# Optimization experiments

Measured on AMD Instinct MI355X. Metric: run time of the kernel, lower is better.

## Reference

```python
import jax, jax.numpy as jnp
import numpy as np

B, S, D = 2048, 200, 192  # batch, seq_len, total_dim
H1, H2 = 64, 32
IN = 4 * D


def prelu(x, a):
    return jnp.where(x >= 0, x, a * x)


def setup_inputs() -> dict:
    key = jax.random.key(0)
    ks = jax.random.split(key, 10)
    scale = lambda fan_in: 1.0 / np.sqrt(fan_in)
    return {
        "query": jax.random.normal(ks[0], (B, D), jnp.float32),
        "keys": jax.random.normal(ks[1], (B, S, D), jnp.float32),
        "keys_mask": jax.random.randint(ks[2], (B, S), 0, 2, jnp.int32),
        "W1": jax.random.uniform(ks[3], (IN, H1), jnp.float32, -scale(IN), scale(IN)),
        "b1": jnp.zeros((H1,), jnp.float32),
        "a1": jnp.asarray(0.25, jnp.float32),  # PReLU default slope
        "W2": jax.random.uniform(ks[4], (H1, H2), jnp.float32, -scale(H1), scale(H1)),
        "b2": jnp.zeros((H2,), jnp.float32),
        "a2": jnp.asarray(0.25, jnp.float32),
        "W3": jax.random.uniform(ks[5], (H2, 1), jnp.float32, -scale(H2), scale(H2)),
        "b3": jnp.zeros((1,), jnp.float32),
    }


def reference(query, keys, keys_mask, W1, b1, a1, W2, b2, a2, W3, b3):
    q = query[:, None, :]  # [B,1,D] broadcasts against keys [B,S,D]
    qe = jnp.broadcast_to(q, keys.shape)
    x = jnp.concatenate([keys, qe, keys * qe, keys - qe], axis=-1)  # [B,S,4D]
    h = prelu(jnp.einsum("bsi,ih->bsh", x, W1) + b1, a1)
    h = prelu(jnp.einsum("bsh,hk->bsk", h, W2) + b2, a2)
    scores = (jnp.einsum("bsk,ko->bso", h, W3) + b3)[..., 0]  # [B,S]
    scores = jnp.where(keys_mask.astype(bool), scores, -jnp.inf)
    w = jax.nn.softmax(scores, axis=-1)
    w = jnp.where(jnp.isnan(w), jnp.zeros_like(w), w)
    weighted_sum = jnp.einsum("bs,bsd->bd", w, keys)
    return weighted_sum, w
```

## Files before the change

kernel.cpp:

```cpp
#include <hip/hip_runtime.h>


#define B_N 2048
#define S_N 200
#define D_N 192

typedef __bf16 bf16x8 __attribute__((ext_vector_type(8)));
typedef __bf16 bf16x4 __attribute__((ext_vector_type(4)));
typedef float  f32x4  __attribute__((ext_vector_type(4)));

struct __align__(16) Smem {
  unsigned char kbuf[64*400];
  unsigned char h1buf[64*144];
  unsigned char w2t[32*144];
  float qbuf[192];
  float cbuf[64];
  float cpart[4][64];
  float scores[256];
  int   maskbuf[256];
  float opart[4][192];
  float wm[4], wl[4];
  float w3buf[32];
  float b2buf[32];
  float consts[4];
};

__global__ __launch_bounds__(256, 3) void rich_attn_kernel(
    const float* __restrict__ query, const float* __restrict__ keys,
    const int*   __restrict__ keys_mask, const float* __restrict__ W1,
    const float* __restrict__ b1, const float* __restrict__ a1,
    const float* __restrict__ W2, const float* __restrict__ b2,
    const float* __restrict__ a2, const float* __restrict__ W3,
    const float* __restrict__ b3, float* __restrict__ out)
{
  __shared__ Smem sm;
  const int tid  = threadIdx.x;
  const int b    = blockIdx.x;
  const int wave = tid >> 6;
  const int lane = tid & 63;
  const int quad = (tid >> 4) & 3;
  const int n16  = tid & 15;

  if (tid < 192) sm.qbuf[tid] = query[b*D_N + tid];
  sm.maskbuf[tid] = (tid < 200) ? keys_mask[b*S_N + tid] : 0;
  if (tid < 32)  sm.w3buf[tid] = W3[tid];
  else if (tid < 64) sm.b2buf[tid-32] = b2[tid-32];
  if (tid == 64) { sm.consts[0] = a1[0]; sm.consts[1] = a2[0]; sm.consts[2] = b3[0]; }
  for (int i = tid; i < 64*32; i += 256) {
    int hh = i >> 5, kk = i & 31;
    *((__bf16*)&sm.w2t[kk*144 + hh*2]) = (__bf16)W2[i];
  }
  __syncthreads();

  {
    int hh = tid & 63, pp = tid >> 6;
    float acc = 0.f;
    int d0 = pp*48;
    #pragma unroll 4
    for (int d = d0; d < d0+48; ++d)
      acc += sm.qbuf[d] * (W1[(192+d)*64 + hh] - W1[(576+d)*64 + hh]);
    sm.cpart[pp][hh] = acc;
  }
  bf16x8 fb1[6];
  {
    int h = (wave << 4) | n16;
    #pragma unroll
    for (int t = 0; t < 6; ++t) {
      #pragma unroll
      for (int j = 0; j < 8; ++j) {
        int d = t*32 + quad*8 + j;
        float v = W1[d*64 + h] + W1[(576+d)*64 + h] + sm.qbuf[d]*W1[(384+d)*64 + h];
        fb1[t][j] = (__bf16)v;
      }
    }
  }
  bf16x8 fw2[2][2];
  #pragma unroll
  for (int nt2 = 0; nt2 < 2; ++nt2)
    #pragma unroll
    for (int t = 0; t < 2; ++t)
      fw2[nt2][t] = *(const bf16x8*)&sm.w2t[(nt2*16 + n16)*144 + (t*32 + quad*8)*2];
  const float w3v0 = sm.w3buf[n16],      w3v1 = sm.w3buf[16 + n16];
  const float bbv0 = sm.b2buf[n16],      bbv1 = sm.b2buf[16 + n16];
  const float a1v = sm.consts[0], a2v = sm.consts[1], b3v = sm.consts[2];
  __syncthreads();
  if (tid < 64)
    sm.cbuf[tid] = b1[tid] + sm.cpart[0][tid] + sm.cpart[1][tid]
                 + sm.cpart[2][tid] + sm.cpart[3][tid];

  const float* kb = keys + (size_t)b * (S_N * D_N);
  float m_run = -1e30f, l_run = 0.f;
  f32x4 o = {0.f, 0.f, 0.f, 0.f};

  for (int tile = 0; tile < 4; ++tile) {
    const int s0 = tile * 64;
    #pragma unroll
    for (int i = 0; i < 12; ++i) {
      int f = tid + i*256;
      int row = f / 48, c4 = f % 48;
      int sg = s0 + row;
      float4 v = make_float4(0.f, 0.f, 0.f, 0.f);
      if (sg < 200) v = ((const float4*)kb)[sg*48 + c4];
      bf16x4 bv; bv[0]=(__bf16)v.x; bv[1]=(__bf16)v.y; bv[2]=(__bf16)v.z; bv[3]=(__bf16)v.w;
      *(bf16x4*)&sm.kbuf[row*400 + c4*8] = bv;
    }
    __syncthreads();

    f32x4 acc1[4];
    #pragma unroll
    for (int mt = 0; mt < 4; ++mt) acc1[mt] = (f32x4){0.f,0.f,0.f,0.f};
    #pragma unroll
    for (int mt = 0; mt < 4; ++mt)
      #pragma unroll
      for (int t = 0; t < 6; ++t) {
        bf16x8 fa = *(const bf16x8*)&sm.kbuf[(mt*16 + n16)*400 + (t*32 + quad*8)*2];
        acc1[mt] = __builtin_amdgcn_mfma_f32_16x16x32_bf16(fa, fb1[t], acc1[mt], 0, 0, 0);
      }
    {
      int h = (wave << 4) | n16;
      float cb = sm.cbuf[h];
      #pragma unroll
      for (int mt = 0; mt < 4; ++mt)
        #pragma unroll
        for (int r = 0; r < 4; ++r) {
          int m = mt*16 + quad*4 + r;
          float v = acc1[mt][r] + cb;
          v = (v >= 0.f) ? v : a1v * v;
          *((__bf16*)&sm.h1buf[m*144 + h*2]) = (__bf16)v;
        }
    }
    __syncthreads();

    bf16x8 fa2[2];
    #pragma unroll
    for (int t = 0; t < 2; ++t)
      fa2[t] = *(const bf16x8*)&sm.h1buf[(wave*16 + n16)*144 + (t*32 + quad*8)*2];
    f32x4 acc2[2];
    acc2[0] = (f32x4){0.f,0.f,0.f,0.f};
    acc2[1] = (f32x4){0.f,0.f,0.f,0.f};
    #pragma unroll
    for (int nt2 = 0; nt2 < 2; ++nt2)
      #pragma unroll
      for (int t = 0; t < 2; ++t)
        acc2[nt2] = __builtin_amdgcn_mfma_f32_16x16x32_bf16(fa2[t], fw2[nt2][t], acc2[nt2], 0, 0, 0);

    float sc[4];
    #pragma unroll
    for (int r = 0; r < 4; ++r) {
      float v0 = acc2[0][r] + bbv0; v0 = (v0 >= 0.f) ? v0 : a2v * v0;
      float v1 = acc2[1][r] + bbv1; v1 = (v1 >= 0.f) ? v1 : a2v * v1;
      sc[r] = v0 * w3v0 + v1 * w3v1;
    }
    #pragma unroll
    for (int off = 1; off < 16; off <<= 1)
      #pragma unroll
      for (int r = 0; r < 4; ++r) sc[r] += __shfl_xor(sc[r], off);

    float p[4];
    float mloc = -1e30f;
    #pragma unroll
    for (int r = 0; r < 4; ++r) {
      int sg = s0 + wave*16 + quad*4 + r;
      sc[r] += b3v;
      bool valid = (sg < 200) && (sm.maskbuf[sg] != 0);
      sc[r] = valid ? sc[r] : -1e30f;
      mloc = fmaxf(mloc, sc[r]);
    }
    if (n16 == 0) {
      #pragma unroll
      for (int r = 0; r < 4; ++r) sm.scores[s0 + wave*16 + quad*4 + r] = sc[r];
    }
    mloc = fmaxf(mloc, __shfl_xor(mloc, 16));
    mloc = fmaxf(mloc, __shfl_xor(mloc, 32));
    float m_new = fmaxf(m_run, mloc);
    float fac = __expf(m_run - m_new);
    float psum = 0.f;
    #pragma unroll
    for (int r = 0; r < 4; ++r) {
      p[r] = (sc[r] > -1e29f) ? __expf(sc[r] - m_new) : 0.f;
      psum += p[r];
    }
    psum += __shfl_xor(psum, 16);
    psum += __shfl_xor(psum, 32);
    l_run = l_run * fac + psum;
    m_run = m_new;

    float pv[16];
    #pragma unroll
    for (int s2 = 0; s2 < 16; ++s2)
      pv[s2] = __shfl(p[s2 & 3], (s2 >> 2) * 16);
    o[0] *= fac; o[1] *= fac; o[2] *= fac; o[3] *= fac;
    if (lane < 48) {
      #pragma unroll
      for (int s2 = 0; s2 < 16; ++s2) {
        bf16x4 kv = *(const bf16x4*)&sm.kbuf[(wave*16 + s2)*400 + lane*8];
        o[0] += pv[s2] * (float)kv[0];
        o[1] += pv[s2] * (float)kv[1];
        o[2] += pv[s2] * (float)kv[2];
        o[3] += pv[s2] * (float)kv[3];
      }
    }
    __syncthreads();
  }

  if (lane == 0) { sm.wm[wave] = m_run; sm.wl[wave] = l_run; }
  if (lane < 48) *(f32x4*)&sm.opart[wave][lane*4] = o;
  __syncthreads();
  float mg = fmaxf(fmaxf(sm.wm[0], sm.wm[1]), fmaxf(sm.wm[2], sm.wm[3]));
  float e0 = __expf(sm.wm[0] - mg), e1 = __expf(sm.wm[1] - mg);
  float e2 = __expf(sm.wm[2] - mg), e3 = __expf(sm.wm[3] - mg);
  float lg = sm.wl[0]*e0 + sm.wl[1]*e1 + sm.wl[2]*e2 + sm.wl[3]*e3;
  float invl = (lg > 0.f) ? 1.f / lg : 0.f;
  if (tid < 192) {
    float os = sm.opart[0][tid]*e0 + sm.opart[1][tid]*e1
             + sm.opart[2][tid]*e2 + sm.opart[3][tid]*e3;
    out[(size_t)b * D_N + tid] = os * invl;
  }
  if (tid < 200) {
    float wv = (lg > 0.f) ? __expf(sm.scores[tid] - mg) * invl : 0.f;
    out[(size_t)B_N * D_N + (size_t)b * S_N + tid] = wv;
  }
}

extern "C" void kernel_launch(void* const* d_in, const int* in_sizes, int n_in,
                              void* d_out, int out_size, void* d_ws, size_t ws_size,
                              hipStream_t stream) {
  const float* query     = (const float*)d_in[0];
  const float* keys      = (const float*)d_in[1];
  const int*   keys_mask = (const int*)  d_in[2];
  const float* W1        = (const float*)d_in[3];
  const float* b1        = (const float*)d_in[4];
  const float* a1        = (const float*)d_in[5];
  const float* W2        = (const float*)d_in[6];
  const float* b2        = (const float*)d_in[7];
  const float* a2        = (const float*)d_in[8];
  const float* W3        = (const float*)d_in[9];
  const float* b3        = (const float*)d_in[10];
  float* out = (float*)d_out;
  rich_attn_kernel<<<dim3(B_N), dim3(256), 0, stream>>>(
      query, keys, keys_mask, W1, b1, a1, W2, b2, a2, W3, b3, out);
}
```

Measured before the change: 548.9 us.

## Double-buffer 32-row key tiles with register prefetch and shrink LDS for occupancy

Splits the sequence into 32-row tiles held in two LDS buffers. The global loads for tile t+2 go into registers while tile t is computed, and the first tile's loads are issued before the weight-preparation prologue. LDS shrinks through unions (h1 with final partials, q/cpart with scores) and a byte mask, and launch bounds rise from 3 to 4 blocks per CU. The aim is to hide global-memory latency that the old load-sync-compute loop exposed. The cost is more loop iterations and barriers, plus half-empty second-layer MFMA tiles (8 valid rows per wave).

```diff
diff --git a/kernel.cpp b/kernel.cpp
--- a/kernel.cpp
+++ b/kernel.cpp
@@ -10,22 +10,24 @@
 typedef float  f32x4  __attribute__((ext_vector_type(4)));
 
 struct __align__(16) Smem {
-  unsigned char kbuf[64*400];
-  unsigned char h1buf[64*144];
-  unsigned char w2t[32*144];
-  float qbuf[192];
+  unsigned char kbuf[2][32*400];
+  union {
+    unsigned char h1buf[32*144];
+    struct { float opart[4][192]; float wm[4]; float wl[4]; } fin;
+  };
+  unsigned char w2t[32*136];
+  union {
+    struct { float qbuf[192]; float cpart[4][64]; } pb;
+    float scores[224];
+  };
   float cbuf[64];
-  float cpart[4][64];
-  float scores[256];
-  int   maskbuf[256];
-  float opart[4][192];
-  float wm[4], wl[4];
+  unsigned char maskbuf[224];
   float w3buf[32];
   float b2buf[32];
   float consts[4];
 };
 
-__global__ __launch_bounds__(256, 3) void rich_attn_kernel(
+__global__ __launch_bounds__(256, 4) void rich_attn_kernel(
     const float* __restrict__ query, const float* __restrict__ keys,
     const int*   __restrict__ keys_mask, const float* __restrict__ W1,
     const float* __restrict__ b1, const float* __restrict__ a1,
@@ -41,14 +43,25 @@
   const int quad = (tid >> 4) & 3;
   const int n16  = tid & 15;
 
-  if (tid < 192) sm.qbuf[tid] = query[b*D_N + tid];
-  sm.maskbuf[tid] = (tid < 200) ? keys_mask[b*S_N + tid] : 0;
+  const float* kb = keys + (size_t)b * (S_N * D_N);
+  const int prow = tid / 8;
+  const int pc4  = (tid & 7);
+
+  float4 pre[6];
+  #pragma unroll
+  for (int i = 0; i < 6; ++i) {
+    int f = tid + i*256, row = f / 48, c4 = f - row*48;
+    pre[i] = ((const float4*)kb)[row*48 + c4];
+  }
+
+  if (tid < 192) sm.pb.qbuf[tid] = query[b*D_N + tid];
+  if (tid < 224) sm.maskbuf[tid] = (tid < 200) ? (unsigned char)(keys_mask[b*S_N + tid] != 0) : 0;
   if (tid < 32)  sm.w3buf[tid] = W3[tid];
   else if (tid < 64) sm.b2buf[tid-32] = b2[tid-32];
   if (tid == 64) { sm.consts[0] = a1[0]; sm.consts[1] = a2[0]; sm.consts[2] = b3[0]; }
   for (int i = tid; i < 64*32; i += 256) {
     int hh = i >> 5, kk = i & 31;
-    *((__bf16*)&sm.w2t[kk*144 + hh*2]) = (__bf16)W2[i];
+    *((__bf16*)&sm.w2t[kk*136 + hh*2]) = (__bf16)W2[i];
   }
   __syncthreads();
 
@@ -58,69 +71,93 @@
     int d0 = pp*48;
     #pragma unroll 4
     for (int d = d0; d < d0+48; ++d)
-      acc += sm.qbuf[d] * (W1[(192+d)*64 + hh] - W1[(576+d)*64 + hh]);
-    sm.cpart[pp][hh] = acc;
+      acc += sm.pb.qbuf[d] * (W1[(192+d)*64 + hh] - W1[(576+d)*64 + hh]);
+    sm.pb.cpart[pp][hh] = acc;
   }
   bf16x8 fb1[6];
   {
     int h = (wave << 4) | n16;
     #pragma unroll
-    for (int t = 0; t < 6; ++t) {
+    for (int t = 0; t < 6; ++t)
       #pragma unroll
       for (int j = 0; j < 8; ++j) {
         int d = t*32 + quad*8 + j;
-        float v = W1[d*64 + h] + W1[(576+d)*64 + h] + sm.qbuf[d]*W1[(384+d)*64 + h];
+        float v = W1[d*64 + h] + W1[(576+d)*64 + h] + sm.pb.qbuf[d]*W1[(384+d)*64 + h];
         fb1[t][j] = (__bf16)v;
       }
-    }
   }
   bf16x8 fw2[2][2];
   #pragma unroll
   for (int nt2 = 0; nt2 < 2; ++nt2)
     #pragma unroll
     for (int t = 0; t < 2; ++t)
-      fw2[nt2][t] = *(const bf16x8*)&sm.w2t[(nt2*16 + n16)*144 + (t*32 + quad*8)*2];
-  const float w3v0 = sm.w3buf[n16],      w3v1 = sm.w3buf[16 + n16];
-  const float bbv0 = sm.b2buf[n16],      bbv1 = sm.b2buf[16 + n16];
+      fw2[nt2][t] = *(const bf16x8*)&sm.w2t[(nt2*16 + n16)*136 + (t*32 + quad*8)*2];
+  const float w3v0 = sm.w3buf[n16], w3v1 = sm.w3buf[16 + n16];
+  const float bbv0 = sm.b2buf[n16], bbv1 = sm.b2buf[16 + n16];
   const float a1v = sm.consts[0], a2v = sm.consts[1], b3v = sm.consts[2];
   __syncthreads();
   if (tid < 64)
-    sm.cbuf[tid] = b1[tid] + sm.cpart[0][tid] + sm.cpart[1][tid]
-                 + sm.cpart[2][tid] + sm.cpart[3][tid];
-
-  const float* kb = keys + (size_t)b * (S_N * D_N);
+    sm.cbuf[tid] = b1[tid] + sm.pb.cpart[0][tid] + sm.pb.cpart[1][tid]
+                 + sm.pb.cpart[2][tid] + sm.pb.cpart[3][tid];
+
+  #pragma unroll
+  for (int i = 0; i < 6; ++i) {
+    int f = tid + i*256, row = f / 48, c4 = f - row*48;
+    float4 v = pre[i];
+    bf16x4 bv; bv[0]=(__bf16)v.x; bv[1]=(__bf16)v.y; bv[2]=(__bf16)v.z; bv[3]=(__bf16)v.w;
+    *(bf16x4*)&sm.kbuf[0][row*400 + c4*8] = bv;
+  }
+  #pragma unroll
+  for (int i = 0; i < 6; ++i) {
+    int f = tid + i*256, row = f / 48, c4 = f - row*48;
+    int sg = 32 + row;
+    pre[i] = ((const float4*)kb)[sg*48 + c4];
+  }
+  __syncthreads();
+
   float m_run = -1e30f, l_run = 0.f;
   f32x4 o = {0.f, 0.f, 0.f, 0.f};
 
-  for (int tile = 0; tile < 4; ++tile) {
-    const int s0 = tile * 64;
-    #pragma unroll
-    for (int i = 0; i < 12; ++i) {
-      int f = tid + i*256;
-      int row = f / 48, c4 = f % 48;
-      int sg = s0 + row;
-      float4 v = make_float4(0.f, 0.f, 0.f, 0.f);
-      if (sg < 200) v = ((const float4*)kb)[sg*48 + c4];
-      bf16x4 bv; bv[0]=(__bf16)v.x; bv[1]=(__bf16)v.y; bv[2]=(__bf16)v.z; bv[3]=(__bf16)v.w;
-      *(bf16x4*)&sm.kbuf[row*400 + c4*8] = bv;
-    }
-    __syncthreads();
-
-    f32x4 acc1[4];
-    #pragma unroll
-    for (int mt = 0; mt < 4; ++mt) acc1[mt] = (f32x4){0.f,0.f,0.f,0.f};
-    #pragma unroll
-    for (int mt = 0; mt < 4; ++mt)
-      #pragma unroll
-      for (int t = 0; t < 6; ++t) {
-        bf16x8 fa = *(const bf16x8*)&sm.kbuf[(mt*16 + n16)*400 + (t*32 + quad*8)*2];
+  for (int tile = 0; tile < 7; ++tile) {
+    const int s0 = tile * 32;
+    const unsigned char* cur = sm.kbuf[tile & 1];
+    unsigned char* nxt = sm.kbuf[(tile + 1) & 1];
+
+    if (tile < 6) {
+      #pragma unroll
+      for (int i = 0; i < 6; ++i) {
+        int f = tid + i*256, row = f / 48, c4 = f - row*48;
+        float4 v = pre[i];
+        bf16x4 bv; bv[0]=(__bf16)v.x; bv[1]=(__bf16)v.y; bv[2]=(__bf16)v.z; bv[3]=(__bf16)v.w;
+        *(bf16x4*)&nxt[row*400 + c4*8] = bv;
+      }
+      if (tile < 5) {
+        #pragma unroll
+        for (int i = 0; i < 6; ++i) {
+          int f = tid + i*256, row = f / 48, c4 = f - row*48;
+          int sg = (tile + 2)*32 + row;
+          float4 v = make_float4(0.f,0.f,0.f,0.f);
+          if (sg < 200) v = ((const float4*)kb)[sg*48 + c4];
+          pre[i] = v;
+        }
+      }
+    }
+
+    f32x4 acc1[2];
+    acc1[0] = (f32x4){0.f,0.f,0.f,0.f};
+    acc1[1] = (f32x4){0.f,0.f,0.f,0.f};
+    #pragma unroll
+    for (int t = 0; t < 6; ++t)
+      #pragma unroll
+      for (int mt = 0; mt < 2; ++mt) {
+        bf16x8 fa = *(const bf16x8*)&cur[(mt*16 + n16)*400 + (t*32 + quad*8)*2];
         acc1[mt] = __builtin_amdgcn_mfma_f32_16x16x32_bf16(fa, fb1[t], acc1[mt], 0, 0, 0);
       }
     {
       int h = (wave << 4) | n16;
       float cb = sm.cbuf[h];
       #pragma unroll
-      for (int mt = 0; mt < 4; ++mt)
+      for (int mt = 0; mt < 2; ++mt)
         #pragma unroll
         for (int r = 0; r < 4; ++r) {
           int m = mt*16 + quad*4 + r;
@@ -134,7 +171,7 @@
     bf16x8 fa2[2];
     #pragma unroll
     for (int t = 0; t < 2; ++t)
-      fa2[t] = *(const bf16x8*)&sm.h1buf[(wave*16 + n16)*144 + (t*32 + quad*8)*2];
+      fa2[t] = *(const bf16x8*)&sm.h1buf[(wave*8 + (n16 & 7))*144 + (t*32 + quad*8)*2];
     f32x4 acc2[2];
     acc2[0] = (f32x4){0.f,0.f,0.f,0.f};
     acc2[1] = (f32x4){0.f,0.f,0.f,0.f};
@@ -160,15 +197,13 @@
     float mloc = -1e30f;
     #pragma unroll
     for (int r = 0; r < 4; ++r) {
-      int sg = s0 + wave*16 + quad*4 + r;
+      int m = quad*4 + r;
+      int sg = s0 + wave*8 + m;
       sc[r] += b3v;
-      bool valid = (sg < 200) && (sm.maskbuf[sg] != 0);
+      bool valid = (m < 8) && (sg < 200) && (sm.maskbuf[sg < 224 ? sg : 0] != 0);
       sc[r] = valid ? sc[r] : -1e30f;
       mloc = fmaxf(mloc, sc[r]);
-    }
-    if (n16 == 0) {
-      #pragma unroll
-      for (int r = 0; r < 4; ++r) sm.scores[s0 + wave*16 + quad*4 + r] = sc[r];
+      if (n16 == 0 && m < 8 && sg < 224) sm.scores[sg] = sc[r];
     }
     mloc = fmaxf(mloc, __shfl_xor(mloc, 16));
     mloc = fmaxf(mloc, __shfl_xor(mloc, 32));
@@ -185,15 +220,15 @@
     l_run = l_run * fac + psum;
     m_run = m_new;
 
-    float pv[16];
-    #pragma unroll
-    for (int s2 = 0; s2 < 16; ++s2)
+    float pv[8];
+    #pragma unroll
+    for (int s2 = 0; s2 < 8; ++s2)
       pv[s2] = __shfl(p[s2 & 3], (s2 >> 2) * 16);
     o[0] *= fac; o[1] *= fac; o[2] *= fac; o[3] *= fac;
     if (lane < 48) {
       #pragma unroll
-      for (int s2 = 0; s2 < 16; ++s2) {
-        bf16x4 kv = *(const bf16x4*)&sm.kbuf[(wave*16 + s2)*400 + lane*8];
+      for (int s2 = 0; s2 < 8; ++s2) {
+        bf16x4 kv = *(const bf16x4*)&cur[(wave*8 + s2)*400 + lane*8];
         o[0] += pv[s2] * (float)kv[0];
         o[1] += pv[s2] * (float)kv[1];
         o[2] += pv[s2] * (float)kv[2];
@@ -203,17 +238,17 @@
     __syncthreads();
   }
 
-  if (lane == 0) { sm.wm[wave] = m_run; sm.wl[wave] = l_run; }
-  if (lane < 48) *(f32x4*)&sm.opart[wave][lane*4] = o;
-  __syncthreads();
-  float mg = fmaxf(fmaxf(sm.wm[0], sm.wm[1]), fmaxf(sm.wm[2], sm.wm[3]));
-  float e0 = __expf(sm.wm[0] - mg), e1 = __expf(sm.wm[1] - mg);
-  float e2 = __expf(sm.wm[2] - mg), e3 = __expf(sm.wm[3] - mg);
-  float lg = sm.wl[0]*e0 + sm.wl[1]*e1 + sm.wl[2]*e2 + sm.wl[3]*e3;
+  if (lane == 0) { sm.fin.wm[wave] = m_run; sm.fin.wl[wave] = l_run; }
+  if (lane < 48) *(f32x4*)&sm.fin.opart[wave][lane*4] = o;
+  __syncthreads();
+  float mg = fmaxf(fmaxf(sm.fin.wm[0], sm.fin.wm[1]), fmaxf(sm.fin.wm[2], sm.fin.wm[3]));
+  float e0 = __expf(sm.fin.wm[0] - mg), e1 = __expf(sm.fin.wm[1] - mg);
+  float e2 = __expf(sm.fin.wm[2] - mg), e3 = __expf(sm.fin.wm[3] - mg);
+  float lg = sm.fin.wl[0]*e0 + sm.fin.wl[1]*e1 + sm.fin.wl[2]*e2 + sm.fin.wl[3]*e3;
   float invl = (lg > 0.f) ? 1.f / lg : 0.f;
   if (tid < 192) {
-    float os = sm.opart[0][tid]*e0 + sm.opart[1][tid]*e1
-             + sm.opart[2][tid]*e2 + sm.opart[3][tid]*e3;
+    float os = sm.fin.opart[0][tid]*e0 + sm.fin.opart[1][tid]*e1
+             + sm.fin.opart[2][tid]*e2 + sm.fin.opart[3][tid]*e3;
     out[(size_t)b * D_N + tid] = os * invl;
   }
   if (tid < 200) {
```

Result: slower. 630.4 us (+14.9%).
